# Kernel optimization log

Hardware: AMD Instinct MI355X
Metric: run time of the kernel (lower is better)

## Reference

```python
import jax, jax.numpy as jnp
import numpy as np

B, L, D, H = 8, 4160, 1024, 16
NB, BL, NS = 64, 64, 64
NT = NB * BL


def setup_inputs() -> dict:
    key = jax.random.key(0)
    ks = jax.random.split(key, 16)
    s = 0.02
    return {
        "query": jax.random.normal(ks[0], (B, L, D), jnp.float32),
        "key": jax.random.normal(ks[1], (B, L, D), jnp.float32),
        "value": jax.random.normal(ks[2], (B, L, D), jnp.float32),
        "temporal_idx": jnp.arange(NT, dtype=jnp.int32),
        "static_idx": jnp.arange(NT, NT + NS, dtype=jnp.int32),
        "temporal_padding_mask": jnp.ones((B, NB, BL), jnp.float32),
        "static_padding_mask": jnp.ones((B, NS), jnp.float32),
        "temporal_shape": (B, NB, BL, D),
        "nhead": H,
        "Wq": s * jax.random.normal(ks[3], (D, D), jnp.float32),
        "bq": jnp.zeros((D,), jnp.float32),
        "Wk": s * jax.random.normal(ks[4], (D, D), jnp.float32),
        "bk": jnp.zeros((D,), jnp.float32),
        "Wv": s * jax.random.normal(ks[5], (D, D), jnp.float32),
        "bv": jnp.zeros((D,), jnp.float32),
        "in_proj_w": s * jax.random.normal(ks[6], (3 * D, D), jnp.float32),
        "in_proj_b": jnp.zeros((3 * D,), jnp.float32),
        "out_w": s * jax.random.normal(ks[7], (D, D), jnp.float32),
        "out_b": jnp.zeros((D,), jnp.float32),
    }


def _mask_bias(m):
    # mask==1 -> keep (0 added), else -inf (matches torch.where(mask==1, 0, -inf))
    return jnp.where(m == 1, 0.0, -jnp.inf)


def _forward(query, key, value, temporal_idx, static_idx, temporal_padding_mask,
             static_padding_mask, temporal_shape, nhead,
             Wq, bq, Wk, bk, Wv, bv, in_proj_w, in_proj_b, out_w, out_b):
    b, nb, bl, d = temporal_shape
    ns = static_idx.shape[0]
    dh = d // nhead
    scale = 1.0 / np.sqrt(dh).astype(np.float32)

    Q = query @ Wq.T + bq
    K = key @ Wk.T + bk
    V = value @ Wv.T + bv

    # ---- temporal side: block-local attention over temporal blocks + global static tokens ----
    Qt = Q[:, temporal_idx].reshape(b, nb, bl, d)
    Ktt = K[:, temporal_idx].reshape(b, nb, bl, d)
    Kts = jnp.broadcast_to(K[:, static_idx][:, None], (b, nb, ns, d))
    Kt = jnp.concatenate([Ktt, Kts], axis=2)                      # [b,nb,bl+ns,d]
    Vtt = V[:, temporal_idx].reshape(b, nb, bl, d)
    Vts = jnp.broadcast_to(V[:, static_idx][:, None], (b, nb, ns, d))
    Vt = jnp.concatenate([Vtt, Vts], axis=2)

    kpm_t = jnp.concatenate(
        [temporal_padding_mask,
         jnp.broadcast_to(static_padding_mask[:, None], (b, nb, ns))], axis=-1)
    bias_t = _mask_bias(kpm_t)                                    # [b,nb,bl+ns]

    Qh = Qt.reshape(b, nb, bl, nhead, dh)
    Kh = Kt.reshape(b, nb, bl + ns, nhead, dh)
    Vh = Vt.reshape(b, nb, bl + ns, nhead, dh)
    logits = jnp.einsum("bnqhd,bnkhd->bhnqk", Qh, Kh) * scale
    logits = logits + bias_t[:, None, :, None, :]
    w = jax.nn.softmax(logits, axis=-1)
    temporal_out = jnp.einsum("bhnqk,bnkhd->bnqhd", w, Vh).reshape(b, nb, bl, d)
    temporal_out = temporal_out.reshape(b, nb * bl, d)

    # ---- static side: full attention (torch.nn.MultiheadAttention with its own projections) ----
    Qs = Q[:, static_idx]                                         # [b,ns,d]
    Ks = jnp.concatenate([K[:, temporal_idx], K[:, static_idx]], axis=1)  # [b,nt+ns,d]
    Vs = jnp.concatenate([V[:, temporal_idx], V[:, static_idx]], axis=1)
    kpm_s = jnp.concatenate([temporal_padding_mask.reshape(b, -1),
                             static_padding_mask], axis=1)        # [b,nt+ns]
    bias_s = _mask_bias(kpm_s)

    q = (Qs @ in_proj_w[:d].T + in_proj_b[:d]).reshape(b, ns, nhead, dh)
    k = (Ks @ in_proj_w[d:2 * d].T + in_proj_b[d:2 * d]).reshape(b, -1, nhead, dh)
    v = (Vs @ in_proj_w[2 * d:].T + in_proj_b[2 * d:]).reshape(b, -1, nhead, dh)
    s_logits = jnp.einsum("bqhd,bkhd->bhqk", q, k) * scale
    s_logits = s_logits + bias_s[:, None, None, :]
    sw = jax.nn.softmax(s_logits, axis=-1)
    static_out = jnp.einsum("bhqk,bkhd->bqhd", sw, v).reshape(b, ns, d)
    static_out = static_out @ out_w.T + out_b

    return jnp.concatenate([temporal_out, static_out], axis=1)    # [b, nt+ns, d]


def reference(query, key, value, temporal_idx, static_idx, temporal_padding_mask,
              static_padding_mask, temporal_shape, nhead,
              Wq, bq, Wk, bk, Wv, bv, in_proj_w, in_proj_b, out_w, out_b):
    return _forward(query, key, value, temporal_idx, static_idx,
                    temporal_padding_mask, static_padding_mask, temporal_shape,
                    nhead, Wq, bq, Wk, bk, Wv, bv, in_proj_w, in_proj_b,
                    out_w, out_b)
```

## Files before the change

kernel.cpp:

```cpp
#include <hip/hip_runtime.h>
#include <hip/hip_bf16.h>
#include <stdint.h>

typedef __bf16 bf16;
typedef bf16 bf16x8 __attribute__((ext_vector_type(8)));
typedef float f32x4 __attribute__((ext_vector_type(4)));

#define MFMA_BF16(a, b, c) __builtin_amdgcn_mfma_f32_16x16x32_bf16((a), (b), (c), 0, 0, 0)

#define BB 8
#define LL 4160
#define DD 1024
#define HH 16
#define NTT 4096
#define NTOK (BB * LL)
#define NSPLIT 13
#define KCHUNK 320

__device__ __forceinline__ f32x4 zero4() {
  f32x4 z = {0.0f, 0.0f, 0.0f, 0.0f};
  return z;
}

typedef __attribute__((address_space(1))) void as1_void;
typedef __attribute__((address_space(3))) void as3_void;

__device__ __forceinline__ void glds16(const void* g, void* l) {
  __builtin_amdgcn_global_load_lds((as1_void*)(uintptr_t)g, (as3_void*)l, 16, 0,
                                   0);
}

__device__ __forceinline__ float loadS(const void* p, size_t idx, int f32) {
  return f32 ? ((const float*)p)[idx] : (float)((const bf16*)p)[idx];
}

__device__ __forceinline__ bf16x8 cvt8(const float* p) {
  const f32x4 a = *(const f32x4*)p;
  const f32x4 b = *(const f32x4*)(p + 4);
  bf16x8 r;
#pragma unroll
  for (int j = 0; j < 4; ++j) {
    r[j] = (bf16)a[j];
    r[j + 4] = (bf16)b[j];
  }
  return r;
}

__device__ __forceinline__ void storeOut8(void* out, size_t idx,
                                          const bf16* src, int f32) {
  if (f32) {
    float* o = (float*)out + idx;
#pragma unroll
    for (int j = 0; j < 8; ++j) o[j] = (float)src[j];
  } else {
    *(bf16x8*)((bf16*)out + idx) = *(const bf16x8*)src;
  }
}

__global__ __launch_bounds__(256) void detect_dtype(
    const unsigned short* __restrict__ q, int* __restrict__ flag) {
  __shared__ int cnt;
  if (threadIdx.x == 0) cnt = 0;
  __syncthreads();
  int c = 0;
  for (int i = threadIdx.x; i < 65536; i += 256) {
    const int e = (q[i] >> 7) & 0xFF;
    c += (e == 0 || e == 0xFF) ? 1 : 0;
  }
  atomicAdd(&cnt, c);
  __syncthreads();
  if (threadIdx.x == 0) *flag = (cnt > 64) ? 1 : 0;
}

__global__ __launch_bounds__(256) void to_bf16(const void* __restrict__ in,
                                               bf16* __restrict__ out, int n8,
                                               const int* __restrict__ dflag) {
  const int f = *dflag;
  const int t = blockIdx.x * 256 + threadIdx.x;
  if (t >= n8) return;
  const size_t idx = (size_t)t * 8;
  if (f) {
    *(bf16x8*)(out + idx) = cvt8((const float*)in + idx);
  } else {
    *(bf16x8*)(out + idx) = *(const bf16x8*)((const bf16*)in + idx);
  }
}

__global__ __launch_bounds__(256) void gemm_bt(
    const void* __restrict__ A, const bf16* __restrict__ W,
    const void* __restrict__ bias, int b_off, bf16* __restrict__ C, int M,
    int N, int K, int ntn, const int* __restrict__ dflag, int a_ext) {
  __shared__ __align__(16) bf16 As[128 * 32];
  __shared__ __align__(16) bf16 Bs[128 * 32];
  const int f = *dflag;
  const int af32 = a_ext ? f : 0;
  const int tid = threadIdx.x;
  const int wave = tid >> 6;
  const int lane = tid & 63;
  const int quad = lane >> 4;
  const int m16 = lane & 15;
  const int bid = (blockIdx.x & 7) * (gridDim.x >> 3) + (blockIdx.x >> 3);
  const int row0 = (bid / ntn) * 128;
  const int col0 = (bid % ntn) * 128;
  const int wm = (wave >> 1) * 64;
  const int wn = (wave & 1) * 64;

  f32x4 acc[4][4];
#pragma unroll
  for (int i = 0; i < 4; ++i)
#pragma unroll
    for (int j = 0; j < 4; ++j) acc[i][j] = zero4();

  const int srow = wave * 32 + (lane >> 2);
  const int scol = (lane & 3) * 8;
  const bf16* Ab = (const bf16*)A;
  const size_t gA0 = (size_t)(row0 + srow) * K + scol;
  const size_t gA1 = gA0 + (size_t)16 * K;
  const size_t gW0 = (size_t)(col0 + srow) * K + scol;
  const size_t gW1 = gW0 + (size_t)16 * K;
  bf16* lA0 = &As[wave * 1024];
  bf16* lA1 = &As[wave * 1024 + 512];
  bf16* lB0 = &Bs[wave * 1024];
  bf16* lB1 = &Bs[wave * 1024 + 512];

  const int sr = tid >> 2;
  const int sc = (tid & 3) * 8;
  const float* Af = (const float*)A;
  const size_t fA0 = (size_t)(row0 + sr) * K + sc;
  const size_t fA1 = (size_t)(row0 + sr + 64) * K + sc;

  for (int kb = 0; kb < K; kb += 32) {
    bf16x8 a0, a1;
    if (af32) {
      a0 = cvt8(Af + fA0 + kb);
      a1 = cvt8(Af + fA1 + kb);
    }
    __syncthreads();
    if (af32) {
      *(bf16x8*)&As[sr * 32 + sc] = a0;
      *(bf16x8*)&As[(sr + 64) * 32 + sc] = a1;
    } else {
      glds16(Ab + gA0 + kb, lA0);
      glds16(Ab + gA1 + kb, lA1);
    }
    glds16(W + gW0 + kb, lB0);
    glds16(W + gW1 + kb, lB1);
    __syncthreads();
    bf16x8 af_[4], bf_[4];
#pragma unroll
    for (int i = 0; i < 4; ++i)
      af_[i] = *(const bf16x8*)&As[(wm + i * 16 + m16) * 32 + quad * 8];
#pragma unroll
    for (int j = 0; j < 4; ++j)
      bf_[j] = *(const bf16x8*)&Bs[(wn + j * 16 + m16) * 32 + quad * 8];
#pragma unroll
    for (int i = 0; i < 4; ++i)
#pragma unroll
      for (int j = 0; j < 4; ++j)
        acc[i][j] = MFMA_BF16(af_[i], bf_[j], acc[i][j]);
  }

#pragma unroll
  for (int j = 0; j < 4; ++j) {
    const int col = col0 + wn + j * 16 + m16;
    const float bv = loadS(bias, b_off + col, f);
#pragma unroll
    for (int i = 0; i < 4; ++i) {
      const int row = row0 + wm + i * 16 + quad * 4;
#pragma unroll
      for (int r = 0; r < 4; ++r)
        C[(size_t)(row + r) * N + col] = (bf16)(acc[i][j][r] + bv);
    }
  }
}

__global__ __launch_bounds__(256) void temporal_attn(
    const bf16* __restrict__ Q, const bf16* __restrict__ K,
    const bf16* __restrict__ V, const void* __restrict__ tmask,
    const void* __restrict__ smask, void* __restrict__ Out,
    const int* __restrict__ dflag) {
  __shared__ __align__(16) char smem[42496];
  bf16* Qs = (bf16*)smem;
  bf16* Ks = (bf16*)(smem + 8192);
  bf16* Vt = (bf16*)(smem + 24576);
  float* biasS = (float*)(smem + 41984);
  bf16* P = (bf16*)smem;
  bf16* Ost = (bf16*)smem;

  const int f = *dflag;
  const int bid = blockIdx.x;
  const int h = bid & 15;
  const int nb = (bid >> 4) & 63;
  const int b = bid >> 10;
  const int tid = threadIdx.x;
  const int wq = tid >> 6;
  const int lane = tid & 63;
  const int quad = lane >> 4;
  const int m16 = lane & 15;

  const size_t tbase = ((size_t)b * LL + nb * 64) * DD + h * 64;
  const size_t sbase = ((size_t)b * LL + NTT) * DD + h * 64;

  {
    const int r = tid >> 3;
    const int cc = (tid & 7) * 8;
    *(bf16x8*)&Qs[r * 64 + cc] = *(const bf16x8*)&Q[tbase + (size_t)r * DD + cc];
    *(bf16x8*)&Qs[(r + 32) * 64 + cc] =
        *(const bf16x8*)&Q[tbase + (size_t)(r + 32) * DD + cc];
    *(bf16x8*)&Ks[r * 64 + cc] = *(const bf16x8*)&K[tbase + (size_t)r * DD + cc];
    *(bf16x8*)&Ks[(r + 32) * 64 + cc] =
        *(const bf16x8*)&K[tbase + (size_t)(r + 32) * DD + cc];
    *(bf16x8*)&Ks[(64 + r) * 64 + cc] =
        *(const bf16x8*)&K[sbase + (size_t)r * DD + cc];
    *(bf16x8*)&Ks[(96 + r) * 64 + cc] =
        *(const bf16x8*)&K[sbase + (size_t)(r + 32) * DD + cc];
  }
#pragma unroll
  for (int t = 0; t < 4; ++t) {
    const int kb = wq * 4 + t;
    bf16x8 tmp;
#pragma unroll
    for (int j = 0; j < 8; ++j) {
      const int kk = kb * 8 + j;
      const size_t rowb = (kk < 64) ? (tbase + (size_t)kk * DD)
                                    : (sbase + (size_t)(kk - 64) * DD);
      tmp[j] = V[rowb + lane];
    }
    *(bf16x8*)&Vt[lane * 136 + kb * 8] = tmp;
  }
  if (tid < 128) {
    const float mv = (tid < 64)
                         ? loadS(tmask, ((size_t)b * 64 + nb) * 64 + tid, f)
                         : loadS(smask, b * 64 + (tid - 64), f);
    biasS[tid] = (mv > 0.5f) ? 0.0f : -1e30f;
  }
  __syncthreads();

  f32x4 s[8];
#pragma unroll
  for (int kt = 0; kt < 8; ++kt) s[kt] = zero4();
#pragma unroll
  for (int ks = 0; ks < 2; ++ks) {
    const bf16x8 aq =
        *(const bf16x8*)&Qs[(wq * 16 + m16) * 64 + ks * 32 + quad * 8];
#pragma unroll
    for (int kt = 0; kt < 8; ++kt) {
      const bf16x8 bk =
          *(const bf16x8*)&Ks[(kt * 16 + m16) * 64 + ks * 32 + quad * 8];
      s[kt] = MFMA_BF16(aq, bk, s[kt]);
    }
  }

  const float scale = 0.125f;
  float invl[4];
#pragma unroll
  for (int r = 0; r < 4; ++r) {
    float mx = -1e30f;
#pragma unroll
    for (int kt = 0; kt < 8; ++kt) {
      float v = s[kt][r] * scale + biasS[kt * 16 + m16];
      s[kt][r] = v;
      mx = fmaxf(mx, v);
    }
#pragma unroll
    for (int off = 1; off < 16; off <<= 1) mx = fmaxf(mx, __shfl_xor(mx, off));
    float sum = 0.0f;
#pragma unroll
    for (int kt = 0; kt < 8; ++kt) {
      float p = __expf(s[kt][r] - mx);
      s[kt][r] = p;
      sum += p;
    }
#pragma unroll
    for (int off = 1; off < 16; off <<= 1) sum += __shfl_xor(sum, off);
    invl[r] = 1.0f / sum;
  }
  __syncthreads();
#pragma unroll
  for (int kt = 0; kt < 8; ++kt)
#pragma unroll
    for (int r = 0; r < 4; ++r)
      P[(wq * 16 + quad * 4 + r) * 136 + kt * 16 + m16] =
          (bf16)(s[kt][r] * invl[r]);

  f32x4 o[4];
#pragma unroll
  for (int j = 0; j < 4; ++j) o[j] = zero4();
#pragma unroll
  for (int ks = 0; ks < 4; ++ks) {
    const bf16x8 ap =
        *(const bf16x8*)&P[(wq * 16 + m16) * 136 + ks * 32 + quad * 8];
#pragma unroll
    for (int j = 0; j < 4; ++j) {
      const bf16x8 bv =
          *(const bf16x8*)&Vt[(j * 16 + m16) * 136 + ks * 32 + quad * 8];
      o[j] = MFMA_BF16(ap, bv, o[j]);
    }
  }
  __syncthreads();
#pragma unroll
  for (int j = 0; j < 4; ++j)
#pragma unroll
    for (int r = 0; r < 4; ++r)
      Ost[(wq * 16 + quad * 4 + r) * 64 + j * 16 + m16] = (bf16)o[j][r];
  __syncthreads();
  {
    const int r = tid >> 3;
    const int cc = (tid & 7) * 8;
    storeOut8(Out, tbase + (size_t)r * DD + cc, &Ost[r * 64 + cc], f);
    storeOut8(Out, tbase + (size_t)(r + 32) * DD + cc, &Ost[(r + 32) * 64 + cc],
              f);
  }
}

__global__ __launch_bounds__(64) void static_attn(
    const bf16* __restrict__ Q2, const bf16* __restrict__ K2,
    const bf16* __restrict__ V2, const void* __restrict__ tmask,
    const void* __restrict__ smask, float* __restrict__ Opart,
    float* __restrict__ Mpart, float* __restrict__ Lpart,
    const int* __restrict__ dflag) {
  __shared__ __align__(16) char smem[34816];
  bf16* Qs = (bf16*)smem;
  bf16* Ks = (bf16*)(smem + 8192);
  bf16* Vt = (bf16*)(smem + 16384);
  bf16* P = (bf16*)(smem + 25600);

  const int f = *dflag;
  const int bid = blockIdx.x;
  const int sp = bid % NSPLIT;
  const int bh = bid / NSPLIT;
  const int h = bh & 15;
  const int b = bh >> 4;
  const int lane = threadIdx.x;
  const int quad = lane >> 4;
  const int m16 = lane & 15;

  {
    const int r = lane >> 3, cc = (lane & 7) * 8;
#pragma unroll
    for (int j = 0; j < 8; ++j) {
      const int rr = j * 8 + r;
      *(bf16x8*)&Qs[rr * 64 + cc] =
          *(const bf16x8*)&Q2[((size_t)(b * 64 + rr)) * DD + h * 64 + cc];
    }
  }

  const float scale = 0.125f;
  float m_run[4][4], l_run[4][4];
  f32x4 o[4][4];
#pragma unroll
  for (int i = 0; i < 4; ++i)
#pragma unroll
    for (int r = 0; r < 4; ++r) {
      m_run[i][r] = -1e30f;
      l_run[i][r] = 0.0f;
    }
#pragma unroll
  for (int i = 0; i < 4; ++i)
#pragma unroll
    for (int j = 0; j < 4; ++j) o[i][j] = zero4();

  const int k0 = sp * KCHUNK;
  for (int t = 0; t < 5; ++t) {
    const int kt0 = k0 + t * 64;
    __syncthreads();
    {
      const int r = lane >> 3, cc = (lane & 7) * 8;
#pragma unroll
      for (int j = 0; j < 8; ++j) {
        const int rr = j * 8 + r;
        *(bf16x8*)&Ks[rr * 64 + cc] =
            *(const bf16x8*)&K2[((size_t)b * LL + kt0 + rr) * DD + h * 64 + cc];
      }
    }
#pragma unroll
    for (int kb = 0; kb < 8; ++kb) {
      bf16x8 tmp;
#pragma unroll
      for (int j = 0; j < 8; ++j)
        tmp[j] = V2[((size_t)b * LL + kt0 + kb * 8 + j) * DD + h * 64 + lane];
      *(bf16x8*)&Vt[lane * 72 + kb * 8] = tmp;
    }
    __syncthreads();

    f32x4 s[4][4];
#pragma unroll
    for (int i = 0; i < 4; ++i)
#pragma unroll
      for (int nt = 0; nt < 4; ++nt) s[i][nt] = zero4();
#pragma unroll
    for (int ks = 0; ks < 2; ++ks) {
      bf16x8 aq[4];
#pragma unroll
      for (int i = 0; i < 4; ++i)
        aq[i] = *(const bf16x8*)&Qs[(i * 16 + m16) * 64 + ks * 32 + quad * 8];
#pragma unroll
      for (int nt = 0; nt < 4; ++nt) {
        const bf16x8 bk =
            *(const bf16x8*)&Ks[(nt * 16 + m16) * 64 + ks * 32 + quad * 8];
#pragma unroll
        for (int i = 0; i < 4; ++i) s[i][nt] = MFMA_BF16(aq[i], bk, s[i][nt]);
      }
    }
    float bias_nt[4];
#pragma unroll
    for (int nt = 0; nt < 4; ++nt) {
      const int kg = kt0 + nt * 16 + m16;
      float mv;
      if (kg < NTT)
        mv = loadS(tmask, (size_t)b * NTT + kg, f);
      else
        mv = loadS(smask, b * 64 + (kg - NTT), f);
      bias_nt[nt] = (mv > 0.5f) ? 0.0f : -1e30f;
    }
#pragma unroll
    for (int i = 0; i < 4; ++i)
#pragma unroll
      for (int r = 0; r < 4; ++r) {
        float mx = -1e30f;
#pragma unroll
        for (int nt = 0; nt < 4; ++nt) {
          float v = s[i][nt][r] * scale + bias_nt[nt];
          s[i][nt][r] = v;
          mx = fmaxf(mx, v);
        }
#pragma unroll
        for (int off = 1; off < 16; off <<= 1)
          mx = fmaxf(mx, __shfl_xor(mx, off));
        const float m_new = fmaxf(m_run[i][r], mx);
        const float alpha = __expf(m_run[i][r] - m_new);
        float sum = 0.0f;
#pragma unroll
        for (int nt = 0; nt < 4; ++nt) {
          float p = __expf(s[i][nt][r] - m_new);
          s[i][nt][r] = p;
          sum += p;
        }
#pragma unroll
        for (int off = 1; off < 16; off <<= 1) sum += __shfl_xor(sum, off);
        l_run[i][r] = l_run[i][r] * alpha + sum;
        m_run[i][r] = m_new;
#pragma unroll
        for (int j = 0; j < 4; ++j) o[i][j][r] *= alpha;
      }
#pragma unroll
    for (int i = 0; i < 4; ++i)
#pragma unroll
      for (int nt = 0; nt < 4; ++nt)
#pragma unroll
        for (int r = 0; r < 4; ++r)
          P[(i * 16 + quad * 4 + r) * 72 + nt * 16 + m16] = (bf16)s[i][nt][r];
    __syncthreads();
#pragma unroll
    for (int ks = 0; ks < 2; ++ks) {
      bf16x8 ap[4], bv[4];
#pragma unroll
      for (int i = 0; i < 4; ++i)
        ap[i] = *(const bf16x8*)&P[(i * 16 + m16) * 72 + ks * 32 + quad * 8];
#pragma unroll
      for (int j = 0; j < 4; ++j)
        bv[j] = *(const bf16x8*)&Vt[(j * 16 + m16) * 72 + ks * 32 + quad * 8];
#pragma unroll
      for (int i = 0; i < 4; ++i)
#pragma unroll
        for (int j = 0; j < 4; ++j) o[i][j] = MFMA_BF16(ap[i], bv[j], o[i][j]);
    }
  }

  const size_t obase = ((size_t)bh * NSPLIT + sp) * 4096;
#pragma unroll
  for (int i = 0; i < 4; ++i)
#pragma unroll
    for (int j = 0; j < 4; ++j)
#pragma unroll
      for (int r = 0; r < 4; ++r)
        Opart[obase + (size_t)(i * 16 + quad * 4 + r) * 64 + j * 16 + m16] =
            o[i][j][r];
  if (m16 == 0) {
    const size_t mbase = ((size_t)bh * NSPLIT + sp) * 64;
#pragma unroll
    for (int i = 0; i < 4; ++i)
#pragma unroll
      for (int r = 0; r < 4; ++r) {
        Mpart[mbase + i * 16 + quad * 4 + r] = m_run[i][r];
        Lpart[mbase + i * 16 + quad * 4 + r] = l_run[i][r];
      }
  }
}

__global__ __launch_bounds__(64) void static_merge(
    const float* __restrict__ Opart, const float* __restrict__ Mpart,
    const float* __restrict__ Lpart, bf16* __restrict__ Sout) {
  const int bh = blockIdx.x;
  const int b = bh >> 4, h = bh & 15;
  const int lane = threadIdx.x;
  for (int r = 0; r < 64; ++r) {
    float M = -1e30f;
    float ms[NSPLIT];
#pragma unroll
    for (int s = 0; s < NSPLIT; ++s) {
      ms[s] = Mpart[((size_t)bh * NSPLIT + s) * 64 + r];
      M = fmaxf(M, ms[s]);
    }
    float L = 0.0f;
    float acc = 0.0f;
#pragma unroll
    for (int s = 0; s < NSPLIT; ++s) {
      const float w = __expf(ms[s] - M);
      L += Lpart[((size_t)bh * NSPLIT + s) * 64 + r] * w;
      acc += w * Opart[(((size_t)bh * NSPLIT + s) * 64 + r) * 64 + lane];
    }
    Sout[((size_t)(b * 64 + r)) * DD + h * 64 + lane] = (bf16)(acc / L);
  }
}

__global__ __launch_bounds__(256) void gather_qs(const bf16* __restrict__ Q,
                                                 bf16* __restrict__ Q2in) {
  const int t = blockIdx.x * 256 + threadIdx.x;
  const int row = t >> 7;
  const int cc = (t & 127) * 8;
  const int b = row >> 6, i = row & 63;
  *(bf16x8*)&Q2in[(size_t)row * DD + cc] =
      *(const bf16x8*)&Q[((size_t)b * LL + NTT + i) * DD + cc];
}

__global__ __launch_bounds__(256) void scatter_out(const bf16* __restrict__ S,
                                                   void* __restrict__ Out,
                                                   const int* __restrict__ dflag) {
  const int f = *dflag;
  const int t = blockIdx.x * 256 + threadIdx.x;
  const int row = t >> 7;
  const int cc = (t & 127) * 8;
  const int b = row >> 6, i = row & 63;
  storeOut8(Out, ((size_t)b * LL + NTT + i) * DD + cc, &S[(size_t)row * DD + cc],
            f);
}

extern "C" void kernel_launch(void* const* d_in, const int* in_sizes, int n_in,
                              void* d_out, int out_size, void* d_ws,
                              size_t ws_size, hipStream_t stream) {
  const void* qkv[3] = {nullptr, nullptr, nullptr};
  const void* W4[4] = {nullptr, nullptr, nullptr, nullptr};
  const void* b4[4] = {nullptr, nullptr, nullptr, nullptr};
  const void *tmask = nullptr, *smask = nullptr, *ipw = nullptr, *ipb = nullptr;
  int nbig = 0, nw = 0, nb_ = 0;
  for (int i = 0; i < n_in; ++i) {
    switch (in_sizes[i]) {
      case 34078720: if (nbig < 3) qkv[nbig++] = d_in[i]; break;
      case 32768: tmask = d_in[i]; break;
      case 512: smask = d_in[i]; break;
      case 1048576: if (nw < 4) W4[nw++] = d_in[i]; break;
      case 1024: if (nb_ < 4) b4[nb_++] = d_in[i]; break;
      case 3145728: ipw = d_in[i]; break;
      case 3072: ipb = d_in[i]; break;
      default: break;
    }
  }

  char* w = (char*)d_ws;
  int* dflag = (int*)w; w += 256;
  const size_t BIG = (size_t)NTOK * DD * 2;
  bf16* Qb = (bf16*)w;  w += BIG;
  bf16* Kb = (bf16*)w;  w += BIG;
  bf16* Vb = (bf16*)w;  w += BIG;
  bf16* Q2in = (bf16*)w;  w += (size_t)512 * DD * 2;
  bf16* Q2 = (bf16*)w;    w += (size_t)512 * DD * 2;
  bf16* SoutB = (bf16*)w; w += (size_t)512 * DD * 2;
  bf16* SoutF = (bf16*)w; w += (size_t)512 * DD * 2;
  float* Opart = (float*)w; w += (size_t)128 * NSPLIT * 4096 * 4;
  float* Mpart = (float*)w; w += (size_t)128 * NSPLIT * 64 * 4;
  float* Lpart = (float*)w; w += (size_t)128 * NSPLIT * 64 * 4;
  bf16* wW3 = (bf16*)w; w += (size_t)1048576 * 2;
  bf16* wW0 = (bf16*)Opart;
  bf16* wW1 = wW0 + 1048576;
  bf16* wW2 = wW1 + 1048576;
  bf16* wIp = wW2 + 1048576;

  detect_dtype<<<1, 256, 0, stream>>>((const unsigned short*)qkv[0], dflag);
  to_bf16<<<512, 256, 0, stream>>>(W4[0], wW0, 131072, dflag);
  to_bf16<<<512, 256, 0, stream>>>(W4[1], wW1, 131072, dflag);
  to_bf16<<<512, 256, 0, stream>>>(W4[2], wW2, 131072, dflag);
  to_bf16<<<512, 256, 0, stream>>>(W4[3], wW3, 131072, dflag);
  to_bf16<<<1536, 256, 0, stream>>>(ipw, wIp, 393216, dflag);
  gemm_bt<<<2080, 256, 0, stream>>>(qkv[0], wW0, b4[0], 0, Qb, NTOK, DD, DD, 8,
                                    dflag, 1);
  gemm_bt<<<2080, 256, 0, stream>>>(qkv[1], wW1, b4[1], 0, Kb, NTOK, DD, DD, 8,
                                    dflag, 1);
  gemm_bt<<<2080, 256, 0, stream>>>(qkv[2], wW2, b4[2], 0, Vb, NTOK, DD, DD, 8,
                                    dflag, 1);
  gather_qs<<<256, 256, 0, stream>>>(Qb, Q2in);
  temporal_attn<<<BB * 64 * HH, 256, 0, stream>>>(Qb, Kb, Vb, tmask, smask,
                                                  d_out, dflag);
  gemm_bt<<<2080, 256, 0, stream>>>(Kb, wIp + (size_t)DD * DD, ipb, DD, Qb,
                                    NTOK, DD, DD, 8, dflag, 0);
  gemm_bt<<<2080, 256, 0, stream>>>(Vb, wIp + (size_t)2 * DD * DD, ipb, 2 * DD,
                                    Kb, NTOK, DD, DD, 8, dflag, 0);
  gemm_bt<<<32, 256, 0, stream>>>(Q2in, wIp, ipb, 0, Q2, 512, DD, DD, 8, dflag,
                                  0);
  static_attn<<<128 * NSPLIT, 64, 0, stream>>>(Q2, Qb, Kb, tmask, smask, Opart,
                                               Mpart, Lpart, dflag);
  static_merge<<<128, 64, 0, stream>>>(Opart, Mpart, Lpart, SoutB);
  gemm_bt<<<32, 256, 0, stream>>>(SoutB, wW3, b4[3], 0, SoutF, 512, DD, DD, 8,
                                  dflag, 0);
  scatter_out<<<256, 256, 0, stream>>>(SoutF, d_out, dflag);
}
```

Baseline: 1.369 ms.

## Triple-buffer GEMM LDS tiles with async prefetch and pre-convert fp32 activations

```diff
diff --git a/kernel.cpp b/kernel.cpp
--- a/kernel.cpp
+++ b/kernel.cpp
@@ -74,8 +74,10 @@
 
 __global__ __launch_bounds__(256) void to_bf16(const void* __restrict__ in,
                                                bf16* __restrict__ out, int n8,
-                                               const int* __restrict__ dflag) {
+                                               const int* __restrict__ dflag,
+                                               int only_f32) {
   const int f = *dflag;
+  if (only_f32 && !f) return;
   const int t = blockIdx.x * 256 + threadIdx.x;
   if (t >= n8) return;
   const size_t idx = (size_t)t * 8;
@@ -87,13 +89,14 @@
 }
 
 __global__ __launch_bounds__(256) void gemm_bt(
-    const void* __restrict__ A, const bf16* __restrict__ W,
-    const void* __restrict__ bias, int b_off, bf16* __restrict__ C, int M,
-    int N, int K, int ntn, const int* __restrict__ dflag, int a_ext) {
-  __shared__ __align__(16) bf16 As[128 * 32];
-  __shared__ __align__(16) bf16 Bs[128 * 32];
+    const void* __restrict__ Aext, const bf16* __restrict__ Astg,
+    const bf16* __restrict__ W, const void* __restrict__ bias, int b_off,
+    bf16* __restrict__ C, int M, int N, int K, int ntn,
+    const int* __restrict__ dflag, int a_ext) {
+  __shared__ __align__(16) bf16 As[3][128 * 32];
+  __shared__ __align__(16) bf16 Bs[3][128 * 32];
   const int f = *dflag;
-  const int af32 = a_ext ? f : 0;
+  const bf16* A = (a_ext && f) ? Astg : (const bf16*)Aext;
   const int tid = threadIdx.x;
   const int wave = tid >> 6;
   const int lane = tid & 63;
@@ -113,52 +116,56 @@
 
   const int srow = wave * 32 + (lane >> 2);
   const int scol = (lane & 3) * 8;
-  const bf16* Ab = (const bf16*)A;
   const size_t gA0 = (size_t)(row0 + srow) * K + scol;
   const size_t gA1 = gA0 + (size_t)16 * K;
   const size_t gW0 = (size_t)(col0 + srow) * K + scol;
   const size_t gW1 = gW0 + (size_t)16 * K;
-  bf16* lA0 = &As[wave * 1024];
-  bf16* lA1 = &As[wave * 1024 + 512];
-  bf16* lB0 = &Bs[wave * 1024];
-  bf16* lB1 = &Bs[wave * 1024 + 512];
-
-  const int sr = tid >> 2;
-  const int sc = (tid & 3) * 8;
-  const float* Af = (const float*)A;
-  const size_t fA0 = (size_t)(row0 + sr) * K + sc;
-  const size_t fA1 = (size_t)(row0 + sr + 64) * K + sc;
-
-  for (int kb = 0; kb < K; kb += 32) {
-    bf16x8 a0, a1;
-    if (af32) {
-      a0 = cvt8(Af + fA0 + kb);
-      a1 = cvt8(Af + fA1 + kb);
-    }
-    __syncthreads();
-    if (af32) {
-      *(bf16x8*)&As[sr * 32 + sc] = a0;
-      *(bf16x8*)&As[(sr + 64) * 32 + sc] = a1;
-    } else {
-      glds16(Ab + gA0 + kb, lA0);
-      glds16(Ab + gA1 + kb, lA1);
-    }
-    glds16(W + gW0 + kb, lB0);
-    glds16(W + gW1 + kb, lB1);
-    __syncthreads();
+
+  const int T = K >> 5;
+
+#define STAGE_TILE(s, t)                                    \
+  do {                                                      \
+    const size_t kb_ = (size_t)(t) << 5;                    \
+    glds16(A + gA0 + kb_, &As[(s)][wave * 1024]);           \
+    glds16(A + gA1 + kb_, &As[(s)][wave * 1024 + 512]);     \
+    glds16(W + gW0 + kb_, &Bs[(s)][wave * 1024]);           \
+    glds16(W + gW1 + kb_, &Bs[(s)][wave * 1024 + 512]);     \
+  } while (0)
+
+  STAGE_TILE(0, 0);
+  STAGE_TILE(1, 1);
+  asm volatile("s_waitcnt vmcnt(4)" ::: "memory");
+  __builtin_amdgcn_s_barrier();
+  __builtin_amdgcn_sched_barrier(0);
+
+  int cur = 0;
+  for (int t = 0; t < T; ++t) {
+    const int pf = t + 2;
+    if (pf < T) {
+      const int s = (cur == 0) ? 2 : cur - 1;
+      STAGE_TILE(s, pf);
+    }
     bf16x8 af_[4], bf_[4];
 #pragma unroll
     for (int i = 0; i < 4; ++i)
-      af_[i] = *(const bf16x8*)&As[(wm + i * 16 + m16) * 32 + quad * 8];
+      af_[i] = *(const bf16x8*)&As[cur][(wm + i * 16 + m16) * 32 + quad * 8];
 #pragma unroll
     for (int j = 0; j < 4; ++j)
-      bf_[j] = *(const bf16x8*)&Bs[(wn + j * 16 + m16) * 32 + quad * 8];
+      bf_[j] = *(const bf16x8*)&Bs[cur][(wn + j * 16 + m16) * 32 + quad * 8];
 #pragma unroll
     for (int i = 0; i < 4; ++i)
 #pragma unroll
       for (int j = 0; j < 4; ++j)
         acc[i][j] = MFMA_BF16(af_[i], bf_[j], acc[i][j]);
-  }
+    if (pf < T)
+      asm volatile("s_waitcnt vmcnt(4)" ::: "memory");
+    else
+      asm volatile("s_waitcnt vmcnt(0)" ::: "memory");
+    __builtin_amdgcn_s_barrier();
+    __builtin_amdgcn_sched_barrier(0);
+    cur = (cur == 2) ? 0 : cur + 1;
+  }
+#undef STAGE_TILE
 
 #pragma unroll
   for (int j = 0; j < 4; ++j) {
@@ -575,32 +582,36 @@
   bf16* wW1 = wW0 + 1048576;
   bf16* wW2 = wW1 + 1048576;
   bf16* wIp = wW2 + 1048576;
+  bf16* Xstg = (bf16*)d_out;
 
   detect_dtype<<<1, 256, 0, stream>>>((const unsigned short*)qkv[0], dflag);
-  to_bf16<<<512, 256, 0, stream>>>(W4[0], wW0, 131072, dflag);
-  to_bf16<<<512, 256, 0, stream>>>(W4[1], wW1, 131072, dflag);
-  to_bf16<<<512, 256, 0, stream>>>(W4[2], wW2, 131072, dflag);
-  to_bf16<<<512, 256, 0, stream>>>(W4[3], wW3, 131072, dflag);
-  to_bf16<<<1536, 256, 0, stream>>>(ipw, wIp, 393216, dflag);
-  gemm_bt<<<2080, 256, 0, stream>>>(qkv[0], wW0, b4[0], 0, Qb, NTOK, DD, DD, 8,
-                                    dflag, 1);
-  gemm_bt<<<2080, 256, 0, stream>>>(qkv[1], wW1, b4[1], 0, Kb, NTOK, DD, DD, 8,
-                                    dflag, 1);
-  gemm_bt<<<2080, 256, 0, stream>>>(qkv[2], wW2, b4[2], 0, Vb, NTOK, DD, DD, 8,
-                                    dflag, 1);
+  to_bf16<<<512, 256, 0, stream>>>(W4[0], wW0, 131072, dflag, 0);
+  to_bf16<<<512, 256, 0, stream>>>(W4[1], wW1, 131072, dflag, 0);
+  to_bf16<<<512, 256, 0, stream>>>(W4[2], wW2, 131072, dflag, 0);
+  to_bf16<<<512, 256, 0, stream>>>(W4[3], wW3, 131072, dflag, 0);
+  to_bf16<<<1536, 256, 0, stream>>>(ipw, wIp, 393216, dflag, 0);
+  to_bf16<<<16640, 256, 0, stream>>>(qkv[0], Xstg, 4259840, dflag, 1);
+  gemm_bt<<<2080, 256, 0, stream>>>(qkv[0], Xstg, wW0, b4[0], 0, Qb, NTOK, DD,
+                                    DD, 8, dflag, 1);
+  to_bf16<<<16640, 256, 0, stream>>>(qkv[1], Xstg, 4259840, dflag, 1);
+  gemm_bt<<<2080, 256, 0, stream>>>(qkv[1], Xstg, wW1, b4[1], 0, Kb, NTOK, DD,
+                                    DD, 8, dflag, 1);
+  to_bf16<<<16640, 256, 0, stream>>>(qkv[2], Xstg, 4259840, dflag, 1);
+  gemm_bt<<<2080, 256, 0, stream>>>(qkv[2], Xstg, wW2, b4[2], 0, Vb, NTOK, DD,
+                                    DD, 8, dflag, 1);
   gather_qs<<<256, 256, 0, stream>>>(Qb, Q2in);
   temporal_attn<<<BB * 64 * HH, 256, 0, stream>>>(Qb, Kb, Vb, tmask, smask,
                                                   d_out, dflag);
-  gemm_bt<<<2080, 256, 0, stream>>>(Kb, wIp + (size_t)DD * DD, ipb, DD, Qb,
+  gemm_bt<<<2080, 256, 0, stream>>>(Kb, Kb, wIp + (size_t)DD * DD, ipb, DD, Qb,
                                     NTOK, DD, DD, 8, dflag, 0);
-  gemm_bt<<<2080, 256, 0, stream>>>(Vb, wIp + (size_t)2 * DD * DD, ipb, 2 * DD,
-                                    Kb, NTOK, DD, DD, 8, dflag, 0);
-  gemm_bt<<<32, 256, 0, stream>>>(Q2in, wIp, ipb, 0, Q2, 512, DD, DD, 8, dflag,
-                                  0);
+  gemm_bt<<<2080, 256, 0, stream>>>(Vb, Vb, wIp + (size_t)2 * DD * DD, ipb,
+                                    2 * DD, Kb, NTOK, DD, DD, 8, dflag, 0);
+  gemm_bt<<<32, 256, 0, stream>>>(Q2in, Q2in, wIp, ipb, 0, Q2, 512, DD, DD, 8,
+                                  dflag, 0);
   static_attn<<<128 * NSPLIT, 64, 0, stream>>>(Q2, Qb, Kb, tmask, smask, Opart,
                                                Mpart, Lpart, dflag);
   static_merge<<<128, 64, 0, stream>>>(Opart, Mpart, Lpart, SoutB);
-  gemm_bt<<<32, 256, 0, stream>>>(SoutB, wW3, b4[3], 0, SoutF, 512, DD, DD, 8,
-                                  dflag, 0);
+  gemm_bt<<<32, 256, 0, stream>>>(SoutB, SoutB, wW3, b4[3], 0, SoutF, 512, DD,
+                                  DD, 8, dflag, 0);
   scatter_out<<<256, 256, 0, stream>>>(SoutF, d_out, dflag);
 }
```

After: 1.257 ms. 8.2% less time.
